# Optimization experiments

Hardware: AMD Instinct MI355X
Metric: run time of the kernel (lower is better)

The kernel has to match this reference:

```python
import jax, jax.numpy as jnp
import numpy as np

NH = 8      # num_heads
DK = 160    # total key/query depth
DV = 64     # total value depth
DKH = DK // NH  # 20
DVH = DV // NH  # 8


def conv2d(x, w, b, pad):
    y = jax.lax.conv_general_dilated(
        x, w, window_strides=(1, 1), padding=[(pad, pad), (pad, pad)],
        dimension_numbers=('NCHW', 'OIHW', 'NCHW'))
    return y + b[None, :, None, None]


def rel_to_abs(x):
    # x: (B, Hd, L, 2L-1) -> (B, Hd, L, L)
    B, Hd, L, _ = x.shape
    x = jnp.pad(x, ((0, 0), (0, 0), (0, 0), (0, 1)))          # (B,Hd,L,2L)
    flat = x.reshape(B, Hd, L * 2 * L)
    flat = jnp.pad(flat, ((0, 0), (0, 0), (0, L - 1)))
    final = flat.reshape(B, Hd, L + 1, 2 * L - 1)
    return final[:, :, :L, L - 1:]


def relative_logits_1d(q, rel_k, H, W, perm):
    # q: (B, NH, H, W, DKH); NOTE: einsum output drops head axis -> sums over heads,
    # exactly as in the torch source ('bhxyd,md->bxym').
    rl = jnp.einsum('bhxyd,md->bxym', q, rel_k)               # (B,H,W,2W-1)
    rl = rel_to_abs(rl.reshape(-1, H, W, 2 * W - 1))          # (B,H,W,W)
    B = rl.shape[0]
    rl = rl[:, None, :, None, :, :]                           # (B,1,H,1,W,W)
    rl = jnp.broadcast_to(rl, (B, NH, H, H, W, W))
    rl = jnp.transpose(rl, perm)
    return rl.reshape(B, NH, H * W, H * W)


def setup_inputs() -> dict:
    key = jax.random.key(0)
    ks = jax.random.split(key, 9)
    s = 0.05
    return {
        'x': jax.random.normal(ks[0], (8, 256, 32, 32), jnp.float32),
        'kqv_w': jax.random.normal(ks[1], (384, 256, 1, 1), jnp.float32) * s,
        'kqv_b': jax.random.normal(ks[2], (384,), jnp.float32) * s,
        'conv_out_w': jax.random.normal(ks[3], (192, 256, 3, 3), jnp.float32) * s,
        'conv_out_b': jax.random.normal(ks[4], (192,), jnp.float32) * s,
        'attn_w': jax.random.normal(ks[5], (64, 64, 1, 1), jnp.float32) * s,
        'attn_b': jax.random.normal(ks[6], (64,), jnp.float32) * s,
        'rel_h': jax.random.normal(ks[7], (63, 20), jnp.float32),
        'rel_w': jax.random.normal(ks[8], (63, 20), jnp.float32),
    }


def reference(x, kqv_w, kqv_b, conv_out_w, conv_out_b, attn_w, attn_b, rel_h, rel_w):
    B, C, H, W = x.shape
    kqv = conv2d(x, kqv_w, kqv_b, 0)
    k, q, v = kqv[:, :DK], kqv[:, DK:2 * DK], kqv[:, 2 * DK:]
    q = q * (DKH ** -0.5)
    # split_heads_2d in the source is a raw reshape (no transpose); replicate exactly
    k = k.reshape(B, NH, H, W, DKH)
    q = q.reshape(B, NH, H, W, DKH)
    v = v.reshape(B, NH, H, W, DVH)
    qf = q.reshape(B, NH, H * W, DKH)
    kf = k.reshape(B, NH, H * W, DKH)
    vf = v.reshape(B, NH, H * W, DVH)
    qk = jnp.einsum('bnid,bnjd->bnij', qf, kf)                # (B,NH,HW,HW)
    qr_w_l = relative_logits_1d(q, rel_w, H, W, (0, 1, 2, 4, 3, 5))
    qr_h_l = relative_logits_1d(jnp.swapaxes(q, 2, 3), rel_h, W, H, (0, 1, 4, 2, 5, 3))
    weights = jax.nn.softmax(qk + qr_h_l + qr_w_l, axis=-1)
    attn = jnp.matmul(weights, vf)                            # (B,NH,HW,DVH)
    attn = attn.reshape(B, NH, DVH, H, W).reshape(B, DV, H, W)  # raw reshapes as in source
    attn = conv2d(attn, attn_w, attn_b, 0)
    return jnp.concatenate([conv2d(x, conv_out_w, conv_out_b, 1), attn], axis=1)
```

## Files before the change

kernel.cpp:

```cpp
#include <hip/hip_runtime.h>

constexpr float QSCALE = 0.22360679774997896f;
constexpr float LOG2E  = 1.4426950408889634f;

typedef __attribute__((ext_vector_type(8))) short bf16x8;
typedef __attribute__((ext_vector_type(4))) float f32x4;

__device__ __forceinline__ unsigned short f2bf(float f) {
    unsigned u = __float_as_uint(f);
    u = (u + 0x7FFFu + ((u >> 16) & 1u)) >> 16;
    return (unsigned short)u;
}

__device__ __forceinline__ unsigned cvt_pk_bf16(float lo, float hi) {
    unsigned r;
    asm("v_cvt_pk_bf16_f32 %0, %1, %2" : "=v"(r) : "v"(lo), "v"(hi));
    return r;
}

__device__ __forceinline__ void qk_decomp(unsigned flat, int& n, int& i, int& d) {
    n = flat / 20480u;
    unsigned r = flat - (unsigned)n * 20480u;
    i = r / 20u;
    d = r - (unsigned)i * 20u;
}

__global__ __launch_bounds__(256) void pack_inputs_kernel(
    const float* __restrict__ X, const float* __restrict__ Wconv,
    const float* __restrict__ Wkqv, const float* __restrict__ Wattn,
    unsigned short* __restrict__ Xt2, unsigned short* __restrict__ Xq,
    unsigned short* __restrict__ Wp, unsigned short* __restrict__ Wq,
    unsigned short* __restrict__ Kb, unsigned short* __restrict__ Qb,
    unsigned short* __restrict__ VtF, unsigned short* __restrict__ Wa)
{
    int t = blockIdx.x * 256 + threadIdx.x;
    if (t < 295936) {
        int b = t / 36992, rem = t - b * 36992;
        int chunk = rem / 4624; int rem2 = rem - chunk * 4624;
        int kc = rem2 / 1156;   int spad = rem2 - kc * 1156;
        int yp = spad / 34, xp = spad - yp * 34;
        bf16x8 v = {};
        if (yp >= 1 && yp <= 32 && xp >= 1 && xp <= 32) {
            const float* src = X + (size_t)b * 262144
                                 + (size_t)(chunk * 32 + kc * 8) * 1024
                                 + (yp - 1) * 32 + (xp - 1);
            #pragma unroll
            for (int j = 0; j < 8; ++j) v[j] = (short)f2bf(src[(size_t)j * 1024]);
        }
        *(bf16x8*)&Xt2[(((size_t)b * 8 + chunk) * 1156 + spad) * 32 + kc * 8] = v;
    } else if (t < 558080) {
        int t2 = t - 295936;
        int lane = t2 & 63;
        int chunk = (t2 >> 6) & 7;
        int g16 = (t2 >> 9) & 63;
        int b = t2 >> 15;
        int sp = g16 * 16 + (lane & 15);
        const float* src = X + (size_t)b * 262144
                             + (size_t)(chunk * 32 + (lane >> 4) * 8) * 1024 + sp;
        bf16x8 v;
        #pragma unroll
        for (int j = 0; j < 8; ++j) v[j] = (short)f2bf(src[(size_t)j * 1024]);
        *(bf16x8*)&Xq[(size_t)t2 * 8] = v;
    } else if (t < 613376) {
        int t2 = t - 558080;
        int l = t2 & 63;
        int rb = (t2 >> 6) & 3;
        int ks = (t2 >> 8) % 72;
        int ot = t2 / 18432;
        int oc = ot * 64 + rb * 16 + (l & 15);
        int kbase = ks * 32 + (l >> 4) * 8;
        bf16x8 v;
        #pragma unroll
        for (int j = 0; j < 8; ++j) {
            int kp = kbase + j;
            int r = kp >> 8, c = kp & 255;
            v[j] = (short)f2bf(Wconv[((size_t)oc * 256 + c) * 9 + r]);
        }
        *(bf16x8*)&Wp[(size_t)t2 * 8] = v;
    } else if (t < 625664) {
        int t2 = t - 613376;
        int l = t2 & 63;
        int rb = (t2 >> 6) & 3;
        int ks = (t2 >> 8) & 7;
        int ot = t2 / 2048;
        int oc = ot * 64 + rb * 16 + (l & 15);
        float sc = (oc >= 160 && oc < 320) ? QSCALE : 1.0f;
        int kbase = ks * 32 + (l >> 4) * 8;
        bf16x8 v;
        #pragma unroll
        for (int j = 0; j < 8; ++j)
            v[j] = (short)f2bf(Wkqv[(size_t)oc * 256 + kbase + j] * sc);
        *(bf16x8*)&Wq[(size_t)t2 * 8] = v;
    } else if (t < 691200) {
        int row = t - 625664;
        bf16x8 z = {};
        *(uint2*)&Kb[(size_t)row * 32 + 20] = make_uint2(0u, 0u);
        *(bf16x8*)&Kb[(size_t)row * 32 + 24] = z;
    } else if (t < 756736) {
        int row = t - 691200;
        bf16x8 z = {};
        *(uint2*)&Qb[(size_t)row * 32 + 20] = make_uint2(0u, 0u);
        *(bf16x8*)&Qb[(size_t)row * 32 + 24] = z;
    } else if (t < 822272) {
        int t2 = t - 756736;
        int bn = t2 >> 10;
        int G = (t2 >> 5) & 31;
        int r8 = (t2 >> 2) & 7;
        int ksub = t2 & 3;
        unsigned short fill = (r8 == 0) ? 0x3F80 : 0;
        bf16x8 v = {short(fill), short(fill), short(fill), short(fill),
                    short(fill), short(fill), short(fill), short(fill)};
        *(bf16x8*)&VtF[(((size_t)bn * 32 + G) * 64 + (8 + r8) + ksub * 16) * 8] = v;
    } else {
        int t2 = t - 822272;
        int l = t2 & 63;
        int rb = (t2 >> 6) & 3;
        int kchunk = t2 >> 8;
        int oc = rb * 16 + (l & 15);
        int kbase = kchunk * 32 + (l >> 4) * 8;
        bf16x8 v;
        #pragma unroll
        for (int j = 0; j < 8; ++j)
            v[j] = (short)f2bf(Wattn[(size_t)oc * 64 + kbase + j]);
        *(bf16x8*)&Wa[(size_t)t2 * 8] = v;
    }
}

__global__ __launch_bounds__(256) void mfma_gemms_kernel(
    const unsigned short* __restrict__ Wp, const unsigned short* __restrict__ Wq,
    const unsigned short* __restrict__ Xt2, const unsigned short* __restrict__ Xq,
    const float* __restrict__ cbias, const float* __restrict__ qbias,
    float* __restrict__ out, float* __restrict__ qf32,
    unsigned short* __restrict__ Kb, unsigned short* __restrict__ Qb,
    unsigned short* __restrict__ VtF)
{
    const int b  = blockIdx.z;
    const int ty = blockIdx.y;
    const int s0 = blockIdx.x * 64;
    const int tid = threadIdx.x;
    const int lane = tid & 63, w = tid >> 6;
    const int wr = w >> 1, wc = w & 1;
    const int kc = lane >> 4, ln = lane & 15;

    f32x4 acc00 = {}, acc01 = {}, acc10 = {}, acc11 = {};
    const int scol = s0 + wc * 32 + ln;

    if (ty < 3) {
        const int Y = blockIdx.x * 2;
        const size_t aoff0 = ((size_t)(ty * 288 + wr * 2) * 64 + lane) * 8;
        const size_t aoff1 = aoff0 + 512;
        const int spad0 = (Y + wc + 1) * 34 + 1 + ln;
        const unsigned short* xb = Xt2 + (size_t)b * 8 * 36992;

        #pragma unroll 1
        for (int cc = 0; cc < 8; ++cc) {
            bf16x8 A0[9], A1[9];
            #pragma unroll
            for (int r = 0; r < 9; ++r) {
                A0[r] = *(const bf16x8*)&Wp[aoff0 + (size_t)(r * 8 + cc) * 2048];
                A1[r] = *(const bf16x8*)&Wp[aoff1 + (size_t)(r * 8 + cc) * 2048];
            }
            const unsigned short* xc = xb + (size_t)cc * 36992 + kc * 8;
            #pragma unroll
            for (int r = 0; r < 9; ++r) {
                const int off = (r / 3 - 1) * 34 + (r % 3 - 1);
                const unsigned short* bp = xc + (size_t)(spad0 + off) * 32;
                bf16x8 b0 = *(const bf16x8*)bp;
                bf16x8 b1 = *(const bf16x8*)(bp + 512);
                acc00 = __builtin_amdgcn_mfma_f32_16x16x32_bf16(A0[r], b0, acc00, 0, 0, 0);
                acc01 = __builtin_amdgcn_mfma_f32_16x16x32_bf16(A0[r], b1, acc01, 0, 0, 0);
                acc10 = __builtin_amdgcn_mfma_f32_16x16x32_bf16(A1[r], b0, acc10, 0, 0, 0);
                acc11 = __builtin_amdgcn_mfma_f32_16x16x32_bf16(A1[r], b1, acc11, 0, 0, 0);
            }
        }

        const int ocb = ty * 64 + wr * 32;
        float* ob = out + (size_t)b * 262144;
        #pragma unroll
        for (int r = 0; r < 4; ++r) {
            int oc0 = ocb + kc * 4 + r;
            float b0v = cbias[oc0];
            ob[(size_t)oc0 * 1024 + scol]      = acc00[r] + b0v;
            ob[(size_t)oc0 * 1024 + scol + 16] = acc01[r] + b0v;
            int oc1 = oc0 + 16;
            float b1v = cbias[oc1];
            ob[(size_t)oc1 * 1024 + scol]      = acc10[r] + b1v;
            ob[(size_t)oc1 * 1024 + scol + 16] = acc11[r] + b1v;
        }
    } else {
        const int ot = ty - 3;
        const size_t aoff0 = ((size_t)(ot * 32 + wr * 2) * 64 + lane) * 8;
        const size_t aoff1 = aoff0 + 512;
        const int g0 = blockIdx.x * 4 + wc * 2;
        const size_t xb0 = (((size_t)b * 64 + g0) * 8) * 512 + lane * 8;
        const size_t xb1 = xb0 + 4096;

        #pragma unroll
        for (int cc = 0; cc < 8; ++cc) {
            bf16x8 a0 = *(const bf16x8*)&Wq[aoff0 + (size_t)cc * 2048];
            bf16x8 a1 = *(const bf16x8*)&Wq[aoff1 + (size_t)cc * 2048];
            bf16x8 b0 = *(const bf16x8*)&Xq[xb0 + (size_t)cc * 512];
            bf16x8 b1 = *(const bf16x8*)&Xq[xb1 + (size_t)cc * 512];
            acc00 = __builtin_amdgcn_mfma_f32_16x16x32_bf16(a0, b0, acc00, 0, 0, 0);
            acc01 = __builtin_amdgcn_mfma_f32_16x16x32_bf16(a0, b1, acc01, 0, 0, 0);
            acc10 = __builtin_amdgcn_mfma_f32_16x16x32_bf16(a1, b0, acc10, 0, 0, 0);
            acc11 = __builtin_amdgcn_mfma_f32_16x16x32_bf16(a1, b1, acc11, 0, 0, 0);
        }

        const int ocb = ot * 64 + wr * 32;
        const int b8 = b * 8;
        #pragma unroll
        for (int r = 0; r < 4; ++r) {
            #pragma unroll
            for (int e = 0; e < 4; ++e) {
                int oc  = ocb + (e >> 1) * 16 + kc * 4 + r;
                int col = scol + (e & 1) * 16;
                float val = (e == 0) ? acc00[r] : (e == 1) ? acc01[r]
                          : (e == 2) ? acc10[r] : acc11[r];
                if (oc < 160) {
                    float v = val + qbias[oc];
                    int n, i, d; qk_decomp((unsigned)oc * 1024u + col, n, i, d);
                    Kb[(((size_t)(b8 + n) * 1024 + i) << 5) + d] = f2bf(v);
                } else if (oc < 320) {
                    float v = val + qbias[oc] * QSCALE;
                    unsigned flat = (unsigned)(oc - 160) * 1024u + col;
                    qf32[(size_t)b * 163840 + flat] = v;
                    int n, i, d; qk_decomp(flat, n, i, d);
                    Qb[(((size_t)(b8 + n) * 1024 + i) << 5) + d] = f2bf(v * LOG2E);
                } else {
                    float v = val + qbias[oc];
                    unsigned flat = (unsigned)(oc - 320) * 1024u + col;
                    int n = flat >> 13, i = (flat >> 3) & 1023, dd = flat & 7;
                    int G = i >> 5, k0 = i & 31;
                    VtF[((((size_t)(b8 + n) * 32 + G) * 64) + dd + ((k0 >> 3) << 4)) * 8
                        + (k0 & 7)] = f2bf(v);
                }
            }
        }
    }
}

__global__ __launch_bounds__(256) void rel_kernel(
    const float* __restrict__ qf32,
    const float* __restrict__ rel_h, const float* __restrict__ rel_w,
    float* __restrict__ Rh, float* __restrict__ Rw)
{
    const int blk = blockIdx.x;
    const int b = blk >> 6, st = blk & 63;
    const int s0 = st * 16;
    const int tid = threadIdx.x;
    __shared__ float rhS[63][21];
    __shared__ float rwS[63][21];
    __shared__ float qs[16][20];

    for (int i = tid; i < 1260; i += 256) {
        int mm = i / 20, d = i - mm * 20;
        rhS[mm][d] = rel_h[i];
        rwS[mm][d] = rel_w[i];
    }
    for (int e = tid; e < 320; e += 256) {
        int s = e / 20, d = e - s * 20;
        const float* qb = qf32 + (size_t)b * 163840 + (s0 + s) * 20 + d;
        float acc = 0.0f;
        #pragma unroll
        for (int n = 0; n < 8; ++n) acc += qb[(size_t)n * 20480];
        qs[s][d] = acc;
    }
    __syncthreads();

    for (int p = tid; p < 1008; p += 256) {
        int s = p / 63, mm = p - s * 63;
        float sh = 0.0f, sw = 0.0f;
        #pragma unroll
        for (int d = 0; d < 20; ++d) {
            float qv = qs[s][d];
            sh += qv * rhS[mm][d];
            sw += qv * rwS[mm][d];
        }
        int sg = s0 + s;
        int y = sg >> 5, x = sg & 31;
        Rw[(size_t)b * 64512 + sg * 63 + mm] = sw * LOG2E;
        Rh[(size_t)b * 64512 + (x * 32 + y) * 63 + mm] = sh * LOG2E;
    }
}

__global__ __launch_bounds__(256, 4) void attn_mfma_kernel(
    const unsigned short* __restrict__ Qb, const unsigned short* __restrict__ Kb,
    const unsigned short* __restrict__ VtF, const float* __restrict__ Rh,
    const float* __restrict__ Rw, float* __restrict__ attnout)
{
    const int bn = blockIdx.y;
    const int b = bn >> 3;
    const int i0 = blockIdx.x * 64;
    const int tid = threadIdx.x;
    const int lane = tid & 63, w = tid >> 6;

    __shared__ float RhS[64][33];
    __shared__ float RwS[64][33];
    __shared__ unsigned short Pl[4][16][72];
    {
        int q = tid & 63, seg = tid >> 6;
        int i = i0 + q, y1 = i >> 5, x1 = i & 31;
        const float* rh = Rh + (size_t)b * 64512 + (x1 * 32 + y1) * 63 + 31 - y1 + seg * 8;
        const float* rw = Rw + (size_t)b * 64512 + i * 63 + 31 - x1 + seg * 8;
        #pragma unroll
        for (int j = 0; j < 8; ++j) {
            RhS[q][seg * 8 + j] = rh[j];
            RwS[q][seg * 8 + j] = rw[j];
        }
    }
    __syncthreads();

    const int ql = lane & 15, g = lane >> 4;
    const int qw = i0 + w * 16;

    bf16x8 qf = *(const bf16x8*)&Qb[((size_t)bn * 1024 + qw + ql) * 32 + g * 8];
    const unsigned short* kp = Kb + ((size_t)bn * 1024 + ql) * 32 + g * 8;
    const unsigned short* vp = VtF + (size_t)bn * 32 * 512 + lane * 8;

    const float* rhrow = &RhS[w * 16 + ql][0];
    float rwA[4], rwB[4];
    #pragma unroll
    for (int r = 0; r < 4; ++r) {
        rwA[r] = RwS[w * 16 + ql][4 * g + r];
        rwB[r] = RwS[w * 16 + ql][16 + 4 * g + r];
    }

    f32x4 oaccT = {};

    bf16x8 c0 = *(const bf16x8*)&kp[0 * 512];
    bf16x8 c1 = *(const bf16x8*)&kp[1 * 512];
    bf16x8 c2 = *(const bf16x8*)&kp[2 * 512];
    bf16x8 c3 = *(const bf16x8*)&kp[3 * 512];

    #pragma unroll 2
    for (int kt = 0; kt < 16; ++kt) {
        __builtin_amdgcn_s_setprio(1);
        f32x4 s0 = {}, s1 = {}, s2 = {}, s3 = {};
        s0 = __builtin_amdgcn_mfma_f32_16x16x32_bf16(c0, qf, s0, 0, 0, 0);
        s1 = __builtin_amdgcn_mfma_f32_16x16x32_bf16(c1, qf, s1, 0, 0, 0);
        s2 = __builtin_amdgcn_mfma_f32_16x16x32_bf16(c2, qf, s2, 0, 0, 0);
        s3 = __builtin_amdgcn_mfma_f32_16x16x32_bf16(c3, qf, s3, 0, 0, 0);
        __builtin_amdgcn_s_setprio(0);

        if (kt < 15) {
            kp += 2048;
            c0 = *(const bf16x8*)&kp[0 * 512];
            c1 = *(const bf16x8*)&kp[1 * 512];
            c2 = *(const bf16x8*)&kp[2 * 512];
            c3 = *(const bf16x8*)&kp[3 * 512];
        }

        float rh0 = rhrow[2 * kt];
        float rh1 = rhrow[2 * kt + 1];

        float p00 = exp2f(s0[0] + rh0 + rwA[0]), p01 = exp2f(s0[1] + rh0 + rwA[1]);
        float p02 = exp2f(s0[2] + rh0 + rwA[2]), p03 = exp2f(s0[3] + rh0 + rwA[3]);
        float p10 = exp2f(s1[0] + rh0 + rwB[0]), p11 = exp2f(s1[1] + rh0 + rwB[1]);
        float p12 = exp2f(s1[2] + rh0 + rwB[2]), p13 = exp2f(s1[3] + rh0 + rwB[3]);
        float p20 = exp2f(s2[0] + rh1 + rwA[0]), p21 = exp2f(s2[1] + rh1 + rwA[1]);
        float p22 = exp2f(s2[2] + rh1 + rwA[2]), p23 = exp2f(s2[3] + rh1 + rwA[3]);
        float p30 = exp2f(s3[0] + rh1 + rwB[0]), p31 = exp2f(s3[1] + rh1 + rwB[1]);
        float p32 = exp2f(s3[2] + rh1 + rwB[2]), p33 = exp2f(s3[3] + rh1 + rwB[3]);

        const int key = 4 * g;
        *(unsigned*)&Pl[w][ql][key]      = cvt_pk_bf16(p00, p01);
        *(unsigned*)&Pl[w][ql][key + 2]  = cvt_pk_bf16(p02, p03);
        *(unsigned*)&Pl[w][ql][key + 16] = cvt_pk_bf16(p10, p11);
        *(unsigned*)&Pl[w][ql][key + 18] = cvt_pk_bf16(p12, p13);
        *(unsigned*)&Pl[w][ql][key + 32] = cvt_pk_bf16(p20, p21);
        *(unsigned*)&Pl[w][ql][key + 34] = cvt_pk_bf16(p22, p23);
        *(unsigned*)&Pl[w][ql][key + 48] = cvt_pk_bf16(p30, p31);
        *(unsigned*)&Pl[w][ql][key + 50] = cvt_pk_bf16(p32, p33);

        #pragma unroll
        for (int half = 0; half < 2; ++half) {
            bf16x8 vfr = *(const bf16x8*)&vp[(size_t)(kt * 2 + half) * 512];
            bf16x8 pfr = *(const bf16x8*)&Pl[w][ql][half * 32 + g * 8];
            __builtin_amdgcn_s_setprio(1);
            oaccT = __builtin_amdgcn_mfma_f32_16x16x32_bf16(vfr, pfr, oaccT, 0, 0, 0);
            __builtin_amdgcn_s_setprio(0);
        }
    }

    float lsum = __shfl(oaccT[0], 32 + ql, 64);
    float inv = 1.0f / lsum;
    if (g < 2) {
        float4 o = {oaccT[0] * inv, oaccT[1] * inv, oaccT[2] * inv, oaccT[3] * inv};
        *(float4*)&attnout[((size_t)bn * 1024 + qw + ql) * 8 + g * 4] = o;
    }
}

__global__ __launch_bounds__(256) void attn_out_mfma_kernel(
    const unsigned short* __restrict__ Wa, const float* __restrict__ attn,
    const float* __restrict__ bias, float* __restrict__ out)
{
    const int b = blockIdx.y;
    const int tid = threadIdx.x;
    const int w = tid >> 6, lane = tid & 63;
    const int sg = blockIdx.x * 4 + w;
    const int kc = lane >> 4, ln = lane & 15;
    const int s = sg * 16 + ln;

    const float* ab = attn + (size_t)b * 65536 + s;

    f32x4 acc0 = {}, acc1 = {}, acc2 = {}, acc3 = {};
    #pragma unroll
    for (int kchunk = 0; kchunk < 2; ++kchunk) {
        const int c0 = kchunk * 32 + kc * 8;
        const float* cp = ab + (size_t)c0 * 1024;
        bf16x8 bf;
        #pragma unroll
        for (int j = 0; j < 8; j += 2) {
            unsigned u = cvt_pk_bf16(cp[(size_t)j * 1024], cp[(size_t)(j + 1) * 1024]);
            bf[j]     = (short)u;
            bf[j + 1] = (short)(u >> 16);
        }

        const unsigned short* wp = Wa + (size_t)kchunk * 2048;
        bf16x8 a0 = *(const bf16x8*)&wp[(size_t)(0 * 64 + lane) * 8];
        bf16x8 a1 = *(const bf16x8*)&wp[(size_t)(1 * 64 + lane) * 8];
        bf16x8 a2 = *(const bf16x8*)&wp[(size_t)(2 * 64 + lane) * 8];
        bf16x8 a3 = *(const bf16x8*)&wp[(size_t)(3 * 64 + lane) * 8];
        acc0 = __builtin_amdgcn_mfma_f32_16x16x32_bf16(a0, bf, acc0, 0, 0, 0);
        acc1 = __builtin_amdgcn_mfma_f32_16x16x32_bf16(a1, bf, acc1, 0, 0, 0);
        acc2 = __builtin_amdgcn_mfma_f32_16x16x32_bf16(a2, bf, acc2, 0, 0, 0);
        acc3 = __builtin_amdgcn_mfma_f32_16x16x32_bf16(a3, bf, acc3, 0, 0, 0);
    }

    float* ob = out + ((size_t)b * 256 + 192) * 1024 + s;
    #pragma unroll
    for (int r = 0; r < 4; ++r) {
        int oc0 = 0 * 16 + kc * 4 + r;
        int oc1 = 1 * 16 + kc * 4 + r;
        int oc2 = 2 * 16 + kc * 4 + r;
        int oc3 = 3 * 16 + kc * 4 + r;
        ob[(size_t)oc0 * 1024] = acc0[r] + bias[oc0];
        ob[(size_t)oc1 * 1024] = acc1[r] + bias[oc1];
        ob[(size_t)oc2 * 1024] = acc2[r] + bias[oc2];
        ob[(size_t)oc3 * 1024] = acc3[r] + bias[oc3];
    }
}

extern "C" void kernel_launch(void* const* d_in, const int* in_sizes, int n_in,
                              void* d_out, int out_size, void* d_ws, size_t ws_size,
                              hipStream_t stream)
{
    const float* x          = (const float*)d_in[0];
    const float* kqv_w      = (const float*)d_in[1];
    const float* kqv_b      = (const float*)d_in[2];
    const float* conv_out_w = (const float*)d_in[3];
    const float* conv_out_b = (const float*)d_in[4];
    const float* attn_w     = (const float*)d_in[5];
    const float* attn_b     = (const float*)d_in[6];
    const float* rel_h      = (const float*)d_in[7];
    const float* rel_w      = (const float*)d_in[8];
    float* out = (float*)d_out;
    float* ws  = (float*)d_ws;

    float* ws_qf32 = ws;
    float* ws_rw   = ws + 1310720;
    float* ws_rh   = ws + 1826816;
    float* ws_attn = ws + 2342912;
    unsigned short* Qb  = (unsigned short*)(ws + 2867200);
    unsigned short* Kb  = (unsigned short*)(ws + 3915776);
    unsigned short* VtF = (unsigned short*)(ws + 4964352);
    unsigned short* Xt2 = (unsigned short*)(ws + 5488640);
    unsigned short* Xq  = (unsigned short*)(ws + 6672384);
    unsigned short* Wp  = (unsigned short*)(ws + 7720960);
    unsigned short* Wq  = (unsigned short*)(ws + 7942144);
    unsigned short* Wa  = (unsigned short*)(ws + 7991296);

    pack_inputs_kernel<<<3214, 256, 0, stream>>>(
        x, conv_out_w, kqv_w, attn_w, Xt2, Xq, Wp, Wq, Kb, Qb, VtF, Wa);
    mfma_gemms_kernel<<<dim3(16, 9, 8), 256, 0, stream>>>(
        Wp, Wq, Xt2, Xq, conv_out_b, kqv_b, out, ws_qf32, Kb, Qb, VtF);
    rel_kernel<<<512, 256, 0, stream>>>(ws_qf32, rel_h, rel_w, ws_rh, ws_rw);
    attn_mfma_kernel<<<dim3(16, 64), 256, 0, stream>>>(
        Qb, Kb, VtF, ws_rh, ws_rw, ws_attn);
    attn_out_mfma_kernel<<<dim3(16, 8), 256, 0, stream>>>(
        Wa, ws_attn, attn_b, out);
}
```

Before: 83.75 us.

## Move 3x3 conv GEMM into attention kernel launch to overlap with attention

Splits the combined GEMM kernel so that only the KQV projection runs before the relative-logits kernel. The 3x3 conv_out GEMM becomes extra blocks (blockIdx.y >= 64) of the attention kernel, so it fills the GPU alongside the attention blocks instead of sitting on the critical path before them. The cost is that the conv blocks now run under the attention kernel's launch bounds and shared-memory allocation, which may limit their occupancy and register use.

```diff
diff --git a/kernel.cpp b/kernel.cpp
--- a/kernel.cpp
+++ b/kernel.cpp
@@ -126,16 +126,14 @@
     }
 }
 
-__global__ __launch_bounds__(256) void mfma_gemms_kernel(
-    const unsigned short* __restrict__ Wp, const unsigned short* __restrict__ Wq,
-    const unsigned short* __restrict__ Xt2, const unsigned short* __restrict__ Xq,
-    const float* __restrict__ cbias, const float* __restrict__ qbias,
-    float* __restrict__ out, float* __restrict__ qf32,
+__global__ __launch_bounds__(256) void mfma_kqv_kernel(
+    const unsigned short* __restrict__ Wq, const unsigned short* __restrict__ Xq,
+    const float* __restrict__ qbias, float* __restrict__ qf32,
     unsigned short* __restrict__ Kb, unsigned short* __restrict__ Qb,
     unsigned short* __restrict__ VtF)
 {
     const int b  = blockIdx.z;
-    const int ty = blockIdx.y;
+    const int ot = blockIdx.y;
     const int s0 = blockIdx.x * 64;
     const int tid = threadIdx.x;
     const int lane = tid & 63, w = tid >> 6;
@@ -145,12 +143,128 @@
     f32x4 acc00 = {}, acc01 = {}, acc10 = {}, acc11 = {};
     const int scol = s0 + wc * 32 + ln;
 
-    if (ty < 3) {
-        const int Y = blockIdx.x * 2;
+    const size_t aoff0 = ((size_t)(ot * 32 + wr * 2) * 64 + lane) * 8;
+    const size_t aoff1 = aoff0 + 512;
+    const int g0 = blockIdx.x * 4 + wc * 2;
+    const size_t xb0 = (((size_t)b * 64 + g0) * 8) * 512 + lane * 8;
+    const size_t xb1 = xb0 + 4096;
+
+    #pragma unroll
+    for (int cc = 0; cc < 8; ++cc) {
+        bf16x8 a0 = *(const bf16x8*)&Wq[aoff0 + (size_t)cc * 2048];
+        bf16x8 a1 = *(const bf16x8*)&Wq[aoff1 + (size_t)cc * 2048];
+        bf16x8 b0 = *(const bf16x8*)&Xq[xb0 + (size_t)cc * 512];
+        bf16x8 b1 = *(const bf16x8*)&Xq[xb1 + (size_t)cc * 512];
+        acc00 = __builtin_amdgcn_mfma_f32_16x16x32_bf16(a0, b0, acc00, 0, 0, 0);
+        acc01 = __builtin_amdgcn_mfma_f32_16x16x32_bf16(a0, b1, acc01, 0, 0, 0);
+        acc10 = __builtin_amdgcn_mfma_f32_16x16x32_bf16(a1, b0, acc10, 0, 0, 0);
+        acc11 = __builtin_amdgcn_mfma_f32_16x16x32_bf16(a1, b1, acc11, 0, 0, 0);
+    }
+
+    const int ocb = ot * 64 + wr * 32;
+    const int b8 = b * 8;
+    #pragma unroll
+    for (int r = 0; r < 4; ++r) {
+        #pragma unroll
+        for (int e = 0; e < 4; ++e) {
+            int oc  = ocb + (e >> 1) * 16 + kc * 4 + r;
+            int col = scol + (e & 1) * 16;
+            float val = (e == 0) ? acc00[r] : (e == 1) ? acc01[r]
+                      : (e == 2) ? acc10[r] : acc11[r];
+            if (oc < 160) {
+                float v = val + qbias[oc];
+                int n, i, d; qk_decomp((unsigned)oc * 1024u + col, n, i, d);
+                Kb[(((size_t)(b8 + n) * 1024 + i) << 5) + d] = f2bf(v);
+            } else if (oc < 320) {
+                float v = val + qbias[oc] * QSCALE;
+                unsigned flat = (unsigned)(oc - 160) * 1024u + col;
+                qf32[(size_t)b * 163840 + flat] = v;
+                int n, i, d; qk_decomp(flat, n, i, d);
+                Qb[(((size_t)(b8 + n) * 1024 + i) << 5) + d] = f2bf(v * LOG2E);
+            } else {
+                float v = val + qbias[oc];
+                unsigned flat = (unsigned)(oc - 320) * 1024u + col;
+                int n = flat >> 13, i = (flat >> 3) & 1023, dd = flat & 7;
+                int G = i >> 5, k0 = i & 31;
+                VtF[((((size_t)(b8 + n) * 32 + G) * 64) + dd + ((k0 >> 3) << 4)) * 8
+                    + (k0 & 7)] = f2bf(v);
+            }
+        }
+    }
+}
+
+__global__ __launch_bounds__(256) void rel_kernel(
+    const float* __restrict__ qf32,
+    const float* __restrict__ rel_h, const float* __restrict__ rel_w,
+    float* __restrict__ Rh, float* __restrict__ Rw)
+{
+    const int blk = blockIdx.x;
+    const int b = blk >> 6, st = blk & 63;
+    const int s0 = st * 16;
+    const int tid = threadIdx.x;
+    __shared__ float rhS[63][21];
+    __shared__ float rwS[63][21];
+    __shared__ float qs[16][20];
+
+    for (int i = tid; i < 1260; i += 256) {
+        int mm = i / 20, d = i - mm * 20;
+        rhS[mm][d] = rel_h[i];
+        rwS[mm][d] = rel_w[i];
+    }
+    for (int e = tid; e < 320; e += 256) {
+        int s = e / 20, d = e - s * 20;
+        const float* qb = qf32 + (size_t)b * 163840 + (s0 + s) * 20 + d;
+        float acc = 0.0f;
+        #pragma unroll
+        for (int n = 0; n < 8; ++n) acc += qb[(size_t)n * 20480];
+        qs[s][d] = acc;
+    }
+    __syncthreads();
+
+    for (int p = tid; p < 1008; p += 256) {
+        int s = p / 63, mm = p - s * 63;
+        float sh = 0.0f, sw = 0.0f;
+        #pragma unroll
+        for (int d = 0; d < 20; ++d) {
+            float qv = qs[s][d];
+            sh += qv * rhS[mm][d];
+            sw += qv * rwS[mm][d];
+        }
+        int sg = s0 + s;
+        int y = sg >> 5, x = sg & 31;
+        Rw[(size_t)b * 64512 + sg * 63 + mm] = sw * LOG2E;
+        Rh[(size_t)b * 64512 + (x * 32 + y) * 63 + mm] = sh * LOG2E;
+    }
+}
+
+__global__ __launch_bounds__(256, 4) void attn_conv_kernel(
+    const unsigned short* __restrict__ Qb, const unsigned short* __restrict__ Kb,
+    const unsigned short* __restrict__ VtF, const float* __restrict__ Rh,
+    const float* __restrict__ Rw, float* __restrict__ attnout,
+    const unsigned short* __restrict__ Wp, const unsigned short* __restrict__ Xt2,
+    const float* __restrict__ cbias, float* __restrict__ out)
+{
+    __shared__ float RhS[64][33];
+    __shared__ float RwS[64][33];
+    __shared__ unsigned short Pl[4][16][72];
+    const int tid = threadIdx.x;
+    const int lane = tid & 63, w = tid >> 6;
+    const int kc = lane >> 4, ln = lane & 15;
+
+    if (blockIdx.y >= 64) {
+        const int t  = blockIdx.y - 64;
+        const int ty = t % 3;
+        const int b  = t / 3;
+        const int s0 = blockIdx.x * 64;
+        const int Y  = blockIdx.x * 2;
+        const int wr = w >> 1, wc = w & 1;
+
         const size_t aoff0 = ((size_t)(ty * 288 + wr * 2) * 64 + lane) * 8;
         const size_t aoff1 = aoff0 + 512;
         const int spad0 = (Y + wc + 1) * 34 + 1 + ln;
         const unsigned short* xb = Xt2 + (size_t)b * 8 * 36992;
+
+        f32x4 acc00 = {}, acc01 = {}, acc10 = {}, acc11 = {};
 
         #pragma unroll 1
         for (int cc = 0; cc < 8; ++cc) {
@@ -175,6 +289,7 @@
         }
 
         const int ocb = ty * 64 + wr * 32;
+        const int scol = s0 + wc * 32 + ln;
         float* ob = out + (size_t)b * 262144;
         #pragma unroll
         for (int r = 0; r < 4; ++r) {
@@ -187,117 +302,12 @@
             ob[(size_t)oc1 * 1024 + scol]      = acc10[r] + b1v;
             ob[(size_t)oc1 * 1024 + scol + 16] = acc11[r] + b1v;
         }
-    } else {
-        const int ot = ty - 3;
-        const size_t aoff0 = ((size_t)(ot * 32 + wr * 2) * 64 + lane) * 8;
-        const size_t aoff1 = aoff0 + 512;
-        const int g0 = blockIdx.x * 4 + wc * 2;
-        const size_t xb0 = (((size_t)b * 64 + g0) * 8) * 512 + lane * 8;
-        const size_t xb1 = xb0 + 4096;
-
-        #pragma unroll
-        for (int cc = 0; cc < 8; ++cc) {
-            bf16x8 a0 = *(const bf16x8*)&Wq[aoff0 + (size_t)cc * 2048];
-            bf16x8 a1 = *(const bf16x8*)&Wq[aoff1 + (size_t)cc * 2048];
-            bf16x8 b0 = *(const bf16x8*)&Xq[xb0 + (size_t)cc * 512];
-            bf16x8 b1 = *(const bf16x8*)&Xq[xb1 + (size_t)cc * 512];
-            acc00 = __builtin_amdgcn_mfma_f32_16x16x32_bf16(a0, b0, acc00, 0, 0, 0);
-            acc01 = __builtin_amdgcn_mfma_f32_16x16x32_bf16(a0, b1, acc01, 0, 0, 0);
-            acc10 = __builtin_amdgcn_mfma_f32_16x16x32_bf16(a1, b0, acc10, 0, 0, 0);
-            acc11 = __builtin_amdgcn_mfma_f32_16x16x32_bf16(a1, b1, acc11, 0, 0, 0);
-        }
-
-        const int ocb = ot * 64 + wr * 32;
-        const int b8 = b * 8;
-        #pragma unroll
-        for (int r = 0; r < 4; ++r) {
-            #pragma unroll
-            for (int e = 0; e < 4; ++e) {
-                int oc  = ocb + (e >> 1) * 16 + kc * 4 + r;
-                int col = scol + (e & 1) * 16;
-                float val = (e == 0) ? acc00[r] : (e == 1) ? acc01[r]
-                          : (e == 2) ? acc10[r] : acc11[r];
-                if (oc < 160) {
-                    float v = val + qbias[oc];
-                    int n, i, d; qk_decomp((unsigned)oc * 1024u + col, n, i, d);
-                    Kb[(((size_t)(b8 + n) * 1024 + i) << 5) + d] = f2bf(v);
-                } else if (oc < 320) {
-                    float v = val + qbias[oc] * QSCALE;
-                    unsigned flat = (unsigned)(oc - 160) * 1024u + col;
-                    qf32[(size_t)b * 163840 + flat] = v;
-                    int n, i, d; qk_decomp(flat, n, i, d);
-                    Qb[(((size_t)(b8 + n) * 1024 + i) << 5) + d] = f2bf(v * LOG2E);
-                } else {
-                    float v = val + qbias[oc];
-                    unsigned flat = (unsigned)(oc - 320) * 1024u + col;
-                    int n = flat >> 13, i = (flat >> 3) & 1023, dd = flat & 7;
-                    int G = i >> 5, k0 = i & 31;
-                    VtF[((((size_t)(b8 + n) * 32 + G) * 64) + dd + ((k0 >> 3) << 4)) * 8
-                        + (k0 & 7)] = f2bf(v);
-                }
-            }
-        }
-    }
-}
-
-__global__ __launch_bounds__(256) void rel_kernel(
-    const float* __restrict__ qf32,
-    const float* __restrict__ rel_h, const float* __restrict__ rel_w,
-    float* __restrict__ Rh, float* __restrict__ Rw)
-{
-    const int blk = blockIdx.x;
-    const int b = blk >> 6, st = blk & 63;
-    const int s0 = st * 16;
-    const int tid = threadIdx.x;
-    __shared__ float rhS[63][21];
-    __shared__ float rwS[63][21];
-    __shared__ float qs[16][20];
-
-    for (int i = tid; i < 1260; i += 256) {
-        int mm = i / 20, d = i - mm * 20;
-        rhS[mm][d] = rel_h[i];
-        rwS[mm][d] = rel_w[i];
-    }
-    for (int e = tid; e < 320; e += 256) {
-        int s = e / 20, d = e - s * 20;
-        const float* qb = qf32 + (size_t)b * 163840 + (s0 + s) * 20 + d;
-        float acc = 0.0f;
-        #pragma unroll
-        for (int n = 0; n < 8; ++n) acc += qb[(size_t)n * 20480];
-        qs[s][d] = acc;
-    }
-    __syncthreads();
-
-    for (int p = tid; p < 1008; p += 256) {
-        int s = p / 63, mm = p - s * 63;
-        float sh = 0.0f, sw = 0.0f;
-        #pragma unroll
-        for (int d = 0; d < 20; ++d) {
-            float qv = qs[s][d];
-            sh += qv * rhS[mm][d];
-            sw += qv * rwS[mm][d];
-        }
-        int sg = s0 + s;
-        int y = sg >> 5, x = sg & 31;
-        Rw[(size_t)b * 64512 + sg * 63 + mm] = sw * LOG2E;
-        Rh[(size_t)b * 64512 + (x * 32 + y) * 63 + mm] = sh * LOG2E;
-    }
-}
-
-__global__ __launch_bounds__(256, 4) void attn_mfma_kernel(
-    const unsigned short* __restrict__ Qb, const unsigned short* __restrict__ Kb,
-    const unsigned short* __restrict__ VtF, const float* __restrict__ Rh,
-    const float* __restrict__ Rw, float* __restrict__ attnout)
-{
+        return;
+    }
+
     const int bn = blockIdx.y;
     const int b = bn >> 3;
     const int i0 = blockIdx.x * 64;
-    const int tid = threadIdx.x;
-    const int lane = tid & 63, w = tid >> 6;
-
-    __shared__ float RhS[64][33];
-    __shared__ float RwS[64][33];
-    __shared__ unsigned short Pl[4][16][72];
     {
         int q = tid & 63, seg = tid >> 6;
         int i = i0 + q, y1 = i >> 5, x1 = i & 31;
@@ -311,7 +321,7 @@
     }
     __syncthreads();
 
-    const int ql = lane & 15, g = lane >> 4;
+    const int ql = ln, g = kc;
     const int qw = i0 + w * 16;
 
     bf16x8 qf = *(const bf16x8*)&Qb[((size_t)bn * 1024 + qw + ql) * 32 + g * 8];
@@ -473,11 +483,11 @@
 
     pack_inputs_kernel<<<3214, 256, 0, stream>>>(
         x, conv_out_w, kqv_w, attn_w, Xt2, Xq, Wp, Wq, Kb, Qb, VtF, Wa);
-    mfma_gemms_kernel<<<dim3(16, 9, 8), 256, 0, stream>>>(
-        Wp, Wq, Xt2, Xq, conv_out_b, kqv_b, out, ws_qf32, Kb, Qb, VtF);
+    mfma_kqv_kernel<<<dim3(16, 6, 8), 256, 0, stream>>>(
+        Wq, Xq, kqv_b, ws_qf32, Kb, Qb, VtF);
     rel_kernel<<<512, 256, 0, stream>>>(ws_qf32, rel_h, rel_w, ws_rh, ws_rw);
-    attn_mfma_kernel<<<dim3(16, 64), 256, 0, stream>>>(
-        Qb, Kb, VtF, ws_rh, ws_rw, ws_attn);
+    attn_conv_kernel<<<dim3(16, 88), 256, 0, stream>>>(
+        Qb, Kb, VtF, ws_rh, ws_rw, ws_attn, Wp, Xt2, conv_out_b, out);
     attn_out_mfma_kernel<<<dim3(16, 8), 256, 0, stream>>>(
         Wa, ws_attn, attn_b, out);
 }
```

New measurement: 84.62 us. Within noise of the previous version (+1.0%).

## Compute head-summed query directly from x in pack kernel, drop rel_kernel launch

Applied to the files above, without the earlier changes.

Because the relative logits sum q over heads, the head-summed weights and bias are precomputed and the summed query is computed straight from x in extra blocks of the pack kernel. This removes the separate rel_kernel launch and the fp32 q write and read from the GEMM kernel. The conv GEMM loop unroll is also raised to 2. The cost is redundant weight summation in every extra block, a 256-long fp32 dot product per element, and a larger shared-memory footprint in the pack kernel, which may lower its occupancy.

```diff
diff --git a/kernel.cpp b/kernel.cpp
--- a/kernel.cpp
+++ b/kernel.cpp
@@ -28,12 +28,79 @@
 __global__ __launch_bounds__(256) void pack_inputs_kernel(
     const float* __restrict__ X, const float* __restrict__ Wconv,
     const float* __restrict__ Wkqv, const float* __restrict__ Wattn,
+    const float* __restrict__ qbias,
+    const float* __restrict__ rel_h, const float* __restrict__ rel_w,
     unsigned short* __restrict__ Xt2, unsigned short* __restrict__ Xq,
     unsigned short* __restrict__ Wp, unsigned short* __restrict__ Wq,
     unsigned short* __restrict__ Kb, unsigned short* __restrict__ Qb,
-    unsigned short* __restrict__ VtF, unsigned short* __restrict__ Wa)
+    unsigned short* __restrict__ VtF, unsigned short* __restrict__ Wa,
+    float* __restrict__ Rh, float* __restrict__ Rw)
 {
-    int t = blockIdx.x * 256 + threadIdx.x;
+    __shared__ float rhS[63][21];
+    __shared__ float rwS[63][21];
+    __shared__ float wsumS[20][260];
+    __shared__ float bsumS[20];
+    __shared__ float qs[16][20];
+    const int tid = threadIdx.x;
+
+    if (blockIdx.x >= 3214) {
+        const int blk = blockIdx.x - 3214;
+        const int b = blk >> 6, st = blk & 63;
+        const int s0 = st * 16;
+
+        for (int i = tid; i < 1260; i += 256) {
+            int mm = i / 20, d = i - mm * 20;
+            rhS[mm][d] = rel_h[i];
+            rwS[mm][d] = rel_w[i];
+        }
+        for (int i = tid; i < 5120; i += 256) {
+            int e = i >> 8, c = i & 255;
+            float s = 0.0f;
+            #pragma unroll
+            for (int n = 0; n < 8; ++n)
+                s += Wkqv[(size_t)(160 + n * 20 + e) * 256 + c];
+            wsumS[e][c] = s;
+        }
+        if (tid < 20) {
+            float s = 0.0f;
+            #pragma unroll
+            for (int n = 0; n < 8; ++n) s += qbias[160 + n * 20 + tid];
+            bsumS[tid] = s;
+        }
+        __syncthreads();
+
+        for (int p = tid; p < 320; p += 256) {
+            int s = p / 20, d = p - s * 20;
+            int flat20 = (s0 + s) * 20 + d;
+            int e   = flat20 >> 10;
+            int col = flat20 & 1023;
+            const float* xp = X + (size_t)b * 262144 + col;
+            float acc = 0.0f;
+            #pragma unroll 4
+            for (int c = 0; c < 256; ++c)
+                acc += wsumS[e][c] * xp[(size_t)c * 1024];
+            qs[s][d] = QSCALE * (acc + bsumS[e]);
+        }
+        __syncthreads();
+
+        for (int p = tid; p < 1008; p += 256) {
+            int s = p / 63, mm = p - s * 63;
+            float sh = 0.0f, sw = 0.0f;
+            #pragma unroll
+            for (int d = 0; d < 20; ++d) {
+                float qv = qs[s][d];
+                sh += qv * rhS[mm][d];
+                sw += qv * rwS[mm][d];
+            }
+            int sg = s0 + s;
+            int y = sg >> 5, x = sg & 31;
+            Rw[(size_t)b * 64512 + sg * 63 + mm] = sw * LOG2E;
+            Rh[(size_t)b * 64512 + (x * 32 + y) * 63 + mm] = sh * LOG2E;
+        }
+        return;
+    }
+
+    int t = blockIdx.x * 256 + tid;
     if (t < 295936) {
         int b = t / 36992, rem = t - b * 36992;
         int chunk = rem / 4624; int rem2 = rem - chunk * 4624;
@@ -130,7 +197,7 @@
     const unsigned short* __restrict__ Wp, const unsigned short* __restrict__ Wq,
     const unsigned short* __restrict__ Xt2, const unsigned short* __restrict__ Xq,
     const float* __restrict__ cbias, const float* __restrict__ qbias,
-    float* __restrict__ out, float* __restrict__ qf32,
+    float* __restrict__ out,
     unsigned short* __restrict__ Kb, unsigned short* __restrict__ Qb,
     unsigned short* __restrict__ VtF)
 {
@@ -152,7 +219,7 @@
         const int spad0 = (Y + wc + 1) * 34 + 1 + ln;
         const unsigned short* xb = Xt2 + (size_t)b * 8 * 36992;
 
-        #pragma unroll 1
+        #pragma unroll 2
         for (int cc = 0; cc < 8; ++cc) {
             bf16x8 A0[9], A1[9];
             #pragma unroll
@@ -224,7 +291,6 @@
                 } else if (oc < 320) {
                     float v = val + qbias[oc] * QSCALE;
                     unsigned flat = (unsigned)(oc - 160) * 1024u + col;
-                    qf32[(size_t)b * 163840 + flat] = v;
                     int n, i, d; qk_decomp(flat, n, i, d);
                     Qb[(((size_t)(b8 + n) * 1024 + i) << 5) + d] = f2bf(v * LOG2E);
                 } else {
@@ -237,50 +303,6 @@
                 }
             }
         }
-    }
-}
-
-__global__ __launch_bounds__(256) void rel_kernel(
-    const float* __restrict__ qf32,
-    const float* __restrict__ rel_h, const float* __restrict__ rel_w,
-    float* __restrict__ Rh, float* __restrict__ Rw)
-{
-    const int blk = blockIdx.x;
-    const int b = blk >> 6, st = blk & 63;
-    const int s0 = st * 16;
-    const int tid = threadIdx.x;
-    __shared__ float rhS[63][21];
-    __shared__ float rwS[63][21];
-    __shared__ float qs[16][20];
-
-    for (int i = tid; i < 1260; i += 256) {
-        int mm = i / 20, d = i - mm * 20;
-        rhS[mm][d] = rel_h[i];
-        rwS[mm][d] = rel_w[i];
-    }
-    for (int e = tid; e < 320; e += 256) {
-        int s = e / 20, d = e - s * 20;
-        const float* qb = qf32 + (size_t)b * 163840 + (s0 + s) * 20 + d;
-        float acc = 0.0f;
-        #pragma unroll
-        for (int n = 0; n < 8; ++n) acc += qb[(size_t)n * 20480];
-        qs[s][d] = acc;
-    }
-    __syncthreads();
-
-    for (int p = tid; p < 1008; p += 256) {
-        int s = p / 63, mm = p - s * 63;
-        float sh = 0.0f, sw = 0.0f;
-        #pragma unroll
-        for (int d = 0; d < 20; ++d) {
-            float qv = qs[s][d];
-            sh += qv * rhS[mm][d];
-            sw += qv * rwS[mm][d];
-        }
-        int sg = s0 + s;
-        int y = sg >> 5, x = sg & 31;
-        Rw[(size_t)b * 64512 + sg * 63 + mm] = sw * LOG2E;
-        Rh[(size_t)b * 64512 + (x * 32 + y) * 63 + mm] = sh * LOG2E;
     }
 }
 
@@ -458,7 +480,6 @@
     float* out = (float*)d_out;
     float* ws  = (float*)d_ws;
 
-    float* ws_qf32 = ws;
     float* ws_rw   = ws + 1310720;
     float* ws_rh   = ws + 1826816;
     float* ws_attn = ws + 2342912;
@@ -471,11 +492,11 @@
     unsigned short* Wq  = (unsigned short*)(ws + 7942144);
     unsigned short* Wa  = (unsigned short*)(ws + 7991296);
 
-    pack_inputs_kernel<<<3214, 256, 0, stream>>>(
-        x, conv_out_w, kqv_w, attn_w, Xt2, Xq, Wp, Wq, Kb, Qb, VtF, Wa);
+    pack_inputs_kernel<<<3726, 256, 0, stream>>>(
+        x, conv_out_w, kqv_w, attn_w, kqv_b, rel_h, rel_w,
+        Xt2, Xq, Wp, Wq, Kb, Qb, VtF, Wa, ws_rh, ws_rw);
     mfma_gemms_kernel<<<dim3(16, 9, 8), 256, 0, stream>>>(
-        Wp, Wq, Xt2, Xq, conv_out_b, kqv_b, out, ws_qf32, Kb, Qb, VtF);
-    rel_kernel<<<512, 256, 0, stream>>>(ws_qf32, rel_h, rel_w, ws_rh, ws_rw);
+        Wp, Wq, Xt2, Xq, conv_out_b, kqv_b, out, Kb, Qb, VtF);
     attn_mfma_kernel<<<dim3(16, 64), 256, 0, stream>>>(
         Qb, Kb, VtF, ws_rh, ws_rw, ws_attn);
     attn_out_mfma_kernel<<<dim3(16, 8), 256, 0, stream>>>(
```

Measured after the change: 139.5 us. +66.6%, slower.
